# Performance work log

Hardware: AMD Instinct MI355X
Metric: run time of the kernel (lower is better)

The kernel has to match this reference:

```python
import jax, jax.numpy as jnp
import numpy as np

EMBED_DIM = 768
NUM_HEADS = 12
HEAD_DIM = EMBED_DIM // NUM_HEADS


def setup_inputs() -> dict:
    key = jax.random.key(0)
    k_x, k_qkv_w, k_qkv_b, k_pw, k_pb = jax.random.split(key, 5)
    B, S = 16, 1024
    scale = 1.0 / np.sqrt(EMBED_DIM)
    return {
        "x": jax.random.normal(k_x, (B, S, EMBED_DIM), dtype=jnp.float32),
        "qkv_w": jax.random.normal(k_qkv_w, (EMBED_DIM, 3 * EMBED_DIM), dtype=jnp.float32) * scale,
        "qkv_b": jax.random.normal(k_qkv_b, (3 * EMBED_DIM,), dtype=jnp.float32) * 0.02,
        "proj_w": jax.random.normal(k_pw, (EMBED_DIM, EMBED_DIM), dtype=jnp.float32) * scale,
        "proj_b": jax.random.normal(k_pb, (EMBED_DIM,), dtype=jnp.float32) * 0.02,
    }


def reference(x, qkv_w, qkv_b, proj_w, proj_b):
    B, S, E = x.shape
    H, D = NUM_HEADS, HEAD_DIM
    qkv = x @ qkv_w + qkv_b                      # [B, S, 3E]
    qkv = qkv.reshape(B, S, 3, H, D)
    qkv = jnp.transpose(qkv, (2, 0, 3, 1, 4))    # [3, B, H, S, D]
    q, k, v = qkv[0], qkv[1], qkv[2]
    scores = jnp.einsum("bhqd,bhkd->bhqk", q, k) / jnp.sqrt(jnp.float32(D))
    probs = jax.nn.softmax(scores, axis=-1)      # dropout is identity in eval
    attn = jnp.einsum("bhqk,bhkd->bhqd", probs, v)
    attn = jnp.transpose(attn, (0, 2, 1, 3)).reshape(B, S, E)
    return attn @ proj_w + proj_b
```

## Files before the change

### kernel.cpp

```cpp
#include <hip/hip_runtime.h>
#include <hip/hip_bf16.h>

typedef unsigned short u16;
typedef unsigned int u32;
typedef short s16x8 __attribute__((ext_vector_type(8)));
typedef float f32x4 __attribute__((ext_vector_type(4)));

#define EMB 768
#define NH 12
#define HD 64
#define BB 16
#define SS 1024
#define MTOK (BB*SS)
#define NQKV (3*EMB)
#define QSZ ((size_t)BB*NH*SS*HD)

#define GLOBAL_AS const __attribute__((address_space(1))) void*
#define LDS_AS __attribute__((address_space(3))) void*

#if __has_builtin(__builtin_amdgcn_exp2f)
#define EXP2(x) __builtin_amdgcn_exp2f(x)
#else
#define EXP2(x) exp2f(x)
#endif

__device__ __forceinline__ u16 f2bf(float f){
  unsigned u = __float_as_uint(f);
  u += 0x7FFFu + ((u >> 16) & 1u);
  return (u16)(u >> 16);
}
__device__ __forceinline__ u16 f2bf_trunc(float f){
  return (u16)(__float_as_uint(f) >> 16);
}
__device__ __forceinline__ f32x4 mfma16(s16x8 a, s16x8 b, f32x4 c){
  return __builtin_amdgcn_mfma_f32_16x16x32_bf16(a, b, c, 0, 0, 0);
}

#define NBA 12288
#define NBB 1728
#define NBC 576

__device__ __forceinline__ void transpose_body(
    u16 (*tile)[33], const float* __restrict__ in, u16* __restrict__ out,
    int R, int C, int bxi, int byi){
  int bx = bxi * 32, by = byi * 32;
  int tx = threadIdx.x & 31, ty = threadIdx.x >> 5;
  #pragma unroll
  for(int i = 0; i < 32; i += 8)
    tile[ty + i][tx] = f2bf(in[(size_t)(by + ty + i) * C + bx + tx]);
  __syncthreads();
  #pragma unroll
  for(int i = 0; i < 32; i += 8)
    out[(size_t)(bx + ty + i) * R + by + tx] = tile[tx][ty + i];
}

__global__ __launch_bounds__(256) void prep_kernel(
    const float4* __restrict__ x4, ushort4* __restrict__ xb4,
    const float* __restrict__ qkv_w, u16* __restrict__ qkv_wT,
    const float* __restrict__ proj_w, u16* __restrict__ proj_wT){
  __shared__ u16 tile[32][33];
  int bid = blockIdx.x;
  if(bid < NBA){
    int i = bid * 256 + threadIdx.x;
    float4 f = x4[i];
    ushort4 o;
    o.x = f2bf(f.x); o.y = f2bf(f.y); o.z = f2bf(f.z); o.w = f2bf(f.w);
    xb4[i] = o;
  } else if(bid < NBA + NBB){
    int bi = bid - NBA;
    transpose_body(tile, qkv_w, qkv_wT, EMB, NQKV, bi % (NQKV/32), bi / (NQKV/32));
  } else {
    int bi = bid - NBA - NBB;
    transpose_body(tile, proj_w, proj_wT, EMB, EMB, bi % (EMB/32), bi / (EMB/32));
  }
}

__global__ __launch_bounds__(256) void qkv_gemm_kernel(
    const u16* __restrict__ A, const u16* __restrict__ Bt,
    const float* __restrict__ bias,
    u16* __restrict__ Qo, u16* __restrict__ Ko, u16* __restrict__ Vo){
  const int K = 768;
  __shared__ u16 SH[4][128*64];
  u16 (*As)[128*64] = &SH[0];
  u16 (*Bs)[128*64] = &SH[2];
  int tid = threadIdx.x;

  int gx = gridDim.x;
  int nwg = gx * gridDim.y;
  int L = blockIdx.y * gx + blockIdx.x;
  int nl = (L & 7) * (nwg >> 3) + (L >> 3);
  int m0 = (nl / gx) * 128, n0 = (nl % gx) * 128;

  int w = tid >> 6, lane = tid & 63, quad = lane >> 4, l15 = lane & 15;
  int wm = (w >> 1) * 64, wn = (w & 1) * 64;
  int rr = lane >> 3;
  int cp = lane & 7;
  f32x4 acc[4][4] = {};

  auto stage = [&](int p, int k0){
    #pragma unroll
    for(int it = 0; it < 4; ++it){
      int ci = it * 4 + w;
      int r  = ci * 8 + rr;
      int gc = (cp ^ (r & 7)) * 8;
      __builtin_amdgcn_global_load_lds(
          (GLOBAL_AS)(A + (size_t)(m0 + r) * K + k0 + gc),
          (LDS_AS)(As[p] + ci * 512 + lane * 8), 16, 0, 0);
      __builtin_amdgcn_global_load_lds(
          (GLOBAL_AS)(Bt + (size_t)(n0 + r) * K + k0 + gc),
          (LDS_AS)(Bs[p] + ci * 512 + lane * 8), 16, 0, 0);
    }
  };

  stage(0, 0);
  int p = 0;
  for(int k0 = 0; k0 < K; k0 += 64){
    __syncthreads();
    if(k0 + 64 < K) stage(p ^ 1, k0 + 64);
    #pragma unroll
    for(int kk = 0; kk < 2; kk++){
      s16x8 a[4], b[4];
      int ch = ((kk * 4 + quad) ^ (l15 & 7)) * 8;
      #pragma unroll
      for(int i = 0; i < 4; i++){
        a[i] = *(const s16x8*)&As[p][(wm + i*16 + l15) * 64 + ch];
        b[i] = *(const s16x8*)&Bs[p][(wn + i*16 + l15) * 64 + ch];
      }
      #pragma unroll
      for(int mt = 0; mt < 4; mt++)
        #pragma unroll
        for(int nt = 0; nt < 4; nt++)
          acc[mt][nt] = mfma16(a[mt], b[nt], acc[mt][nt]);
    }
    p ^= 1;
  }

  int which = (n0 + wn) / EMB;
  if(which == 2){
    #pragma unroll
    for(int mt = 0; mt < 4; mt++){
      #pragma unroll
      for(int nt = 0; nt < 4; nt++){
        int n = n0 + wn + nt*16 + l15;
        float bv = bias[n];
        int rem = n - 2 * EMB;
        int h = rem >> 6, d = rem & 63;
        int mbase = m0 + wm + mt*16 + quad*4;
        int bb = mbase >> 10, sb = mbase & 1023;
        size_t bh = (size_t)(bb * NH + h);
        ushort4 pk;
        pk.x = f2bf(acc[mt][nt][0] + bv);
        pk.y = f2bf(acc[mt][nt][1] + bv);
        pk.z = f2bf(acc[mt][nt][2] + bv);
        pk.w = f2bf(acc[mt][nt][3] + bv);
        *(ushort4*)&Vo[(bh * HD + d) * SS + sb] = pk;
      }
    }
  } else {
    u16* ep = &SH[0][0];
    __syncthreads();
    #pragma unroll
    for(int mt = 0; mt < 4; mt++){
      #pragma unroll
      for(int nt = 0; nt < 4; nt++){
        int n = n0 + wn + nt*16 + l15;
        float bv = bias[n];
        int row0 = wm + mt*16 + quad*4;
        #pragma unroll
        for(int r = 0; r < 4; r++)
          ep[(row0 + r) * 136 + wn + nt*16 + l15] = f2bf(acc[mt][nt][r] + bv);
      }
    }
    __syncthreads();
    u16* dst = (which == 0) ? Qo : Ko;
    int nb = n0 - which * EMB;
    #pragma unroll
    for(int pass = 0; pass < 8; ++pass){
      int c = pass * 256 + tid;
      int row = c >> 4, chunk = c & 15;
      s16x8 v = *(const s16x8*)&ep[row * 136 + chunk * 8];
      int m = m0 + row;
      int bb = m >> 10, ss = m & 1023;
      int rem = nb + chunk * 8;
      int h = rem >> 6, d = rem & 63;
      size_t bh = (size_t)(bb * NH + h);
      *(s16x8*)&dst[(bh * SS + ss) * HD + d] = v;
    }
  }
}

__global__ __launch_bounds__(512, 2) void proj_gemm_kernel(
    const u16* __restrict__ A, const u16* __restrict__ Bt,
    const float* __restrict__ bias, float* __restrict__ out){
  const int K = 768, NT = 12;
  __shared__ u16 As[2][256*64];
  __shared__ u16 Bs[2][256*64];
  int tid = threadIdx.x;

  int gx = gridDim.x;
  int nwg = gx * gridDim.y;
  int L = blockIdx.y * gx + blockIdx.x;
  int nl = (L & 7) * (nwg >> 3) + (L >> 3);
  int m0 = (nl / gx) * 256, n0 = (nl % gx) * 256;

  int w = tid >> 6, lane = tid & 63, quad = lane >> 4, l15 = lane & 15;
  int wm = (w >> 2) * 128, wn = (w & 3) * 64;
  int rr = lane >> 3;
  int cp = lane & 7;
  f32x4 acc[8][4] = {};

  auto stageQ = [&](int t, int q){
    int d = t & 1, k0 = t * 64;
    const u16* src = (q < 2) ? A : Bt;
    int base = (q < 2) ? m0 : n0;
    u16* dst = (q < 2) ? As[d] : Bs[d];
    int h = q & 1;
    #pragma unroll
    for(int it = 0; it < 2; ++it){
      int ci = h*16 + it*8 + w;
      int r  = ci * 8 + rr;
      int gc = (cp ^ (r & 7)) * 8;
      __builtin_amdgcn_global_load_lds(
          (GLOBAL_AS)(src + (size_t)(base + r) * K + k0 + gc),
          (LDS_AS)(dst + ci * 512 + lane * 8), 16, 0, 0);
    }
  };

  s16x8 a[8], b0[4], b1[4];
  auto dsA = [&](int d, int mh){
    #pragma unroll
    for(int kk = 0; kk < 2; ++kk){
      int ch = ((kk*4 + quad) ^ (l15 & 7)) * 8;
      #pragma unroll
      for(int i = 0; i < 4; ++i)
        a[kk*4+i] = *(const s16x8*)&As[d][(wm + (mh*4+i)*16 + l15) * 64 + ch];
    }
  };
  auto dsB = [&](int d, int nh, s16x8* bb){
    #pragma unroll
    for(int kk = 0; kk < 2; ++kk){
      int ch = ((kk*4 + quad) ^ (l15 & 7)) * 8;
      #pragma unroll
      for(int j = 0; j < 2; ++j)
        bb[kk*2+j] = *(const s16x8*)&Bs[d][(wn + (nh*2+j)*16 + l15) * 64 + ch];
    }
  };
  auto mfmaQ = [&](int mh, int nh, const s16x8* bb){
    __builtin_amdgcn_s_setprio(1);
    #pragma unroll
    for(int kk = 0; kk < 2; ++kk)
      #pragma unroll
      for(int i = 0; i < 4; ++i)
        #pragma unroll
        for(int j = 0; j < 2; ++j)
          acc[mh*4+i][nh*2+j] = mfma16(a[kk*4+i], bb[kk*2+j], acc[mh*4+i][nh*2+j]);
    __builtin_amdgcn_s_setprio(0);
  };

#define PHASE_SYNC() do{ \
    __builtin_amdgcn_s_barrier(); \
    asm volatile("s_waitcnt lgkmcnt(0)" ::: "memory"); \
    __builtin_amdgcn_sched_barrier(0); \
  }while(0)
#define PHASE_END() do{ \
    __builtin_amdgcn_s_barrier(); \
    __builtin_amdgcn_sched_barrier(0); \
  }while(0)

  stageQ(0,0); stageQ(0,1); stageQ(0,2); stageQ(0,3);
  stageQ(1,0);
  asm volatile("s_waitcnt vmcnt(2)" ::: "memory");
  __builtin_amdgcn_s_barrier();
  __builtin_amdgcn_sched_barrier(0);

  #pragma unroll
  for(int j = 0; j < NT/2; ++j){
    int t = 2*j;
    stageQ(t+1, 1);
    dsA(0, 0); dsB(0, 0, b0);
    PHASE_SYNC(); mfmaQ(0, 0, b0); PHASE_END();
    stageQ(t+1, 2);
    dsB(0, 1, b1);
    PHASE_SYNC(); mfmaQ(0, 1, b1); PHASE_END();
    stageQ(t+1, 3);
    dsA(0, 1);
    PHASE_SYNC(); mfmaQ(1, 0, b0); PHASE_END();
    if(t+2 < NT){ stageQ(t+2, 0); asm volatile("s_waitcnt vmcnt(2)" ::: "memory"); }
    else        { asm volatile("s_waitcnt vmcnt(0)" ::: "memory"); }
    PHASE_SYNC(); mfmaQ(1, 1, b1); PHASE_END();
    if(t+2 < NT) stageQ(t+2, 1);
    dsA(1, 0); dsB(1, 0, b0);
    PHASE_SYNC(); mfmaQ(0, 0, b0); PHASE_END();
    if(t+2 < NT) stageQ(t+2, 2);
    dsB(1, 1, b1);
    PHASE_SYNC(); mfmaQ(0, 1, b1); PHASE_END();
    if(t+2 < NT) stageQ(t+2, 3);
    dsA(1, 1);
    PHASE_SYNC(); mfmaQ(1, 0, b0); PHASE_END();
    if(t+3 < NT){ stageQ(t+3, 0); asm volatile("s_waitcnt vmcnt(2)" ::: "memory"); }
    else if(t+2 < NT){ asm volatile("s_waitcnt vmcnt(0)" ::: "memory"); }
    PHASE_SYNC(); mfmaQ(1, 1, b1); PHASE_END();
  }
#undef PHASE_SYNC
#undef PHASE_END

  #pragma unroll
  for(int mt = 0; mt < 8; ++mt){
    #pragma unroll
    for(int nt = 0; nt < 4; ++nt){
      int n = n0 + wn + nt*16 + l15;
      float bv = bias[n];
      #pragma unroll
      for(int r = 0; r < 4; ++r){
        int m = m0 + wm + mt*16 + quad*4 + r;
        out[(size_t)m * EMB + n] = acc[mt][nt][r] + bv;
      }
    }
  }
}

__global__ __launch_bounds__(512) void attn_kernel(
    const u16* __restrict__ Qws, const u16* __restrict__ Kws,
    const u16* __restrict__ Vtws, u16* __restrict__ attn){
  __shared__ u16 Ks[2][64*64];
  __shared__ u16 Vs[2][64*64];
  __shared__ __align__(16) u16 Ps[8][2][16][76];
  int tid = threadIdx.x;
  int w = tid >> 6, lane = tid & 63, quad = lane >> 4, l15 = lane & 15;
  int bh = blockIdx.x;
  int b = bh / NH, h = bh - b * NH;
  int q0 = blockIdx.y * 256 + w * 32;
  const u16* Qbase = Qws  + (size_t)bh * SS * HD;
  const u16* Kbase = Kws  + (size_t)bh * SS * HD;
  const u16* Vbase = Vtws + (size_t)bh * HD * SS;

  s16x8 aq[2][2];
  #pragma unroll
  for(int m = 0; m < 2; m++){
    int qrow = q0 + m*16 + l15;
    #pragma unroll
    for(int kk = 0; kk < 2; kk++)
      aq[m][kk] = *(const s16x8*)(Qbase + (size_t)qrow * HD + kk*32 + quad*8);
  }

  f32x4 o[2][4] = {};
  float psum[2][4] = {};
  const float C1 = 0.125f * 1.44269504f;
  const float C0 = -30.0f * 1.44269504f;

  int krr = lane >> 3, kcp = lane & 7;

  auto stageKV = [&](int p, int kt){
    int ins = w;
    int r   = ins * 8 + krr;
    int gck = (kcp ^ (r & 7)) * 8;
    __builtin_amdgcn_global_load_lds(
        (GLOBAL_AS)(Kbase + (size_t)(kt*64 + r) * HD + gck),
        (LDS_AS)(Ks[p] + ins * 512 + lane * 8), 16, 0, 0);
    __builtin_amdgcn_global_load_lds(
        (GLOBAL_AS)(Vbase + (size_t)r * SS + kt*64 + gck),
        (LDS_AS)(Vs[p] + ins * 512 + lane * 8), 16, 0, 0);
  };

  stageKV(0, 0);
  int p = 0;
  for(int kt = 0; kt < 16; ++kt){
    __syncthreads();
    if(kt < 15) stageKV(p ^ 1, kt + 1);

    #pragma unroll
    for(int nt = 0; nt < 4; ++nt){
      s16x8 bk[2];
      #pragma unroll
      for(int kk = 0; kk < 2; kk++){
        int ch = ((kk*4 + quad) ^ (l15 & 7)) * 8;
        bk[kk] = *(const s16x8*)&Ks[p][(nt*16 + l15) * 64 + ch];
      }
      #pragma unroll
      for(int m = 0; m < 2; m++){
        f32x4 z = {};
        z = mfma16(aq[m][0], bk[0], z);
        z = mfma16(aq[m][1], bk[1], z);
        #pragma unroll
        for(int r = 0; r < 4; r++){
          float pv = EXP2(z[r] * C1 + C0);
          psum[m][r] += pv;
          Ps[w][m][quad*4 + r][nt*16 + l15] = f2bf_trunc(pv);
        }
      }
    }
    #pragma unroll
    for(int k4 = 0; k4 < 2; k4++){
      s16x8 pa[2];
      #pragma unroll
      for(int m = 0; m < 2; m++)
        pa[m] = *(const s16x8*)&Ps[w][m][l15][k4*32 + quad*8];
      #pragma unroll
      for(int nt = 0; nt < 4; nt++){
        int ch = ((k4*4 + quad) ^ (l15 & 7)) * 8;
        s16x8 vb = *(const s16x8*)&Vs[p][(nt*16 + l15) * 64 + ch];
        #pragma unroll
        for(int m = 0; m < 2; m++)
          o[m][nt] = mfma16(pa[m], vb, o[m][nt]);
      }
    }
    p ^= 1;
  }

  #pragma unroll
  for(int m = 0; m < 2; m++){
    #pragma unroll
    for(int r = 0; r < 4; r++){
      float s = psum[m][r];
      s += __shfl_xor(s, 1, 64);
      s += __shfl_xor(s, 2, 64);
      s += __shfl_xor(s, 4, 64);
      s += __shfl_xor(s, 8, 64);
      float inv = 1.0f / s;
      int srow = q0 + m*16 + quad*4 + r;
      size_t base = ((size_t)(b * SS + srow)) * EMB + h * HD;
      #pragma unroll
      for(int nt = 0; nt < 4; nt++)
        attn[base + nt*16 + l15] = f2bf(o[m][nt][r] * inv);
    }
  }
}

extern "C" void kernel_launch(void* const* d_in, const int* in_sizes, int n_in,
                              void* d_out, int out_size, void* d_ws, size_t ws_size,
                              hipStream_t stream){
  const float* x      = (const float*)d_in[0];
  const float* qkv_w  = (const float*)d_in[1];
  const float* qkv_b  = (const float*)d_in[2];
  const float* proj_w = (const float*)d_in[3];
  const float* proj_b = (const float*)d_in[4];

  char* ws = (char*)d_ws;
  u16* qkv_wT  = (u16*)ws; ws += (size_t)NQKV * EMB * 2;
  u16* proj_wT = (u16*)ws; ws += (size_t)EMB * EMB * 2;
  u16* x_bf = (u16*)ws; ws += QSZ * 2;
  u16* Qws  = (u16*)ws; ws += QSZ * 2;
  u16* Kws  = (u16*)ws; ws += QSZ * 2;
  u16* Vtws = (u16*)ws; ws += QSZ * 2;
  u16* attn = x_bf;

  prep_kernel<<<NBA + NBB + NBC, 256, 0, stream>>>(
      (const float4*)x, (ushort4*)x_bf, qkv_w, qkv_wT, proj_w, proj_wT);
  qkv_gemm_kernel<<<dim3(NQKV/128, MTOK/128), 256, 0, stream>>>(
      x_bf, qkv_wT, qkv_b, Qws, Kws, Vtws);
  attn_kernel<<<dim3(BB*NH, SS/256), 512, 0, stream>>>(Qws, Kws, Vtws, attn);
  proj_gemm_kernel<<<dim3(EMB/256, MTOK/256), 512, 0, stream>>>(
      attn, proj_wT, proj_b, (float*)d_out);
}
```

Measured before the change: 277.0 us.

## Shrink proj GEMM to 128x128 tiles with simple double buffer and LDS-staged epilogue

Replaces the 256x256, 512-thread proj GEMM, which used a hand-scheduled 8-phase pipeline, with a 128x128, 256-thread kernel. The new kernel uses a plain double-buffered K loop. The output is staged through LDS in two halves so each fp32 row is written to global memory with coalesced float4 stores. The aim is more workgroups for better CU occupancy and wave balance (768 tiles instead of 192) and cheaper scattered stores. In exchange it loses the finer MFMA/load interleaving and reuses less data per tile.

```diff
diff --git a/kernel.cpp b/kernel.cpp
--- a/kernel.cpp
+++ b/kernel.cpp
@@ -189,132 +189,90 @@
   }
 }
 
-__global__ __launch_bounds__(512, 2) void proj_gemm_kernel(
+__global__ __launch_bounds__(256) void proj_gemm_kernel(
     const u16* __restrict__ A, const u16* __restrict__ Bt,
     const float* __restrict__ bias, float* __restrict__ out){
-  const int K = 768, NT = 12;
-  __shared__ u16 As[2][256*64];
-  __shared__ u16 Bs[2][256*64];
+  const int K = 768;
+  __shared__ u16 SH[4][128*64];
+  u16 (*As)[128*64] = &SH[0];
+  u16 (*Bs)[128*64] = &SH[2];
   int tid = threadIdx.x;
 
   int gx = gridDim.x;
   int nwg = gx * gridDim.y;
   int L = blockIdx.y * gx + blockIdx.x;
   int nl = (L & 7) * (nwg >> 3) + (L >> 3);
-  int m0 = (nl / gx) * 256, n0 = (nl % gx) * 256;
+  int m0 = (nl / gx) * 128, n0 = (nl % gx) * 128;
 
   int w = tid >> 6, lane = tid & 63, quad = lane >> 4, l15 = lane & 15;
-  int wm = (w >> 2) * 128, wn = (w & 3) * 64;
+  int wm = (w >> 1) * 64, wn = (w & 1) * 64;
   int rr = lane >> 3;
   int cp = lane & 7;
-  f32x4 acc[8][4] = {};
-
-  auto stageQ = [&](int t, int q){
-    int d = t & 1, k0 = t * 64;
-    const u16* src = (q < 2) ? A : Bt;
-    int base = (q < 2) ? m0 : n0;
-    u16* dst = (q < 2) ? As[d] : Bs[d];
-    int h = q & 1;
-    #pragma unroll
-    for(int it = 0; it < 2; ++it){
-      int ci = h*16 + it*8 + w;
+  f32x4 acc[4][4] = {};
+
+  auto stage = [&](int p, int k0){
+    #pragma unroll
+    for(int it = 0; it < 4; ++it){
+      int ci = it * 4 + w;
       int r  = ci * 8 + rr;
       int gc = (cp ^ (r & 7)) * 8;
       __builtin_amdgcn_global_load_lds(
-          (GLOBAL_AS)(src + (size_t)(base + r) * K + k0 + gc),
-          (LDS_AS)(dst + ci * 512 + lane * 8), 16, 0, 0);
+          (GLOBAL_AS)(A + (size_t)(m0 + r) * K + k0 + gc),
+          (LDS_AS)(As[p] + ci * 512 + lane * 8), 16, 0, 0);
+      __builtin_amdgcn_global_load_lds(
+          (GLOBAL_AS)(Bt + (size_t)(n0 + r) * K + k0 + gc),
+          (LDS_AS)(Bs[p] + ci * 512 + lane * 8), 16, 0, 0);
     }
   };
 
-  s16x8 a[8], b0[4], b1[4];
-  auto dsA = [&](int d, int mh){
-    #pragma unroll
-    for(int kk = 0; kk < 2; ++kk){
-      int ch = ((kk*4 + quad) ^ (l15 & 7)) * 8;
-      #pragma unroll
-      for(int i = 0; i < 4; ++i)
-        a[kk*4+i] = *(const s16x8*)&As[d][(wm + (mh*4+i)*16 + l15) * 64 + ch];
-    }
-  };
-  auto dsB = [&](int d, int nh, s16x8* bb){
-    #pragma unroll
-    for(int kk = 0; kk < 2; ++kk){
-      int ch = ((kk*4 + quad) ^ (l15 & 7)) * 8;
-      #pragma unroll
-      for(int j = 0; j < 2; ++j)
-        bb[kk*2+j] = *(const s16x8*)&Bs[d][(wn + (nh*2+j)*16 + l15) * 64 + ch];
-    }
-  };
-  auto mfmaQ = [&](int mh, int nh, const s16x8* bb){
-    __builtin_amdgcn_s_setprio(1);
-    #pragma unroll
-    for(int kk = 0; kk < 2; ++kk)
-      #pragma unroll
-      for(int i = 0; i < 4; ++i)
-        #pragma unroll
-        for(int j = 0; j < 2; ++j)
-          acc[mh*4+i][nh*2+j] = mfma16(a[kk*4+i], bb[kk*2+j], acc[mh*4+i][nh*2+j]);
-    __builtin_amdgcn_s_setprio(0);
-  };
-
-#define PHASE_SYNC() do{ \
-    __builtin_amdgcn_s_barrier(); \
-    asm volatile("s_waitcnt lgkmcnt(0)" ::: "memory"); \
-    __builtin_amdgcn_sched_barrier(0); \
-  }while(0)
-#define PHASE_END() do{ \
-    __builtin_amdgcn_s_barrier(); \
-    __builtin_amdgcn_sched_barrier(0); \
-  }while(0)
-
-  stageQ(0,0); stageQ(0,1); stageQ(0,2); stageQ(0,3);
-  stageQ(1,0);
-  asm volatile("s_waitcnt vmcnt(2)" ::: "memory");
-  __builtin_amdgcn_s_barrier();
-  __builtin_amdgcn_sched_barrier(0);
-
+  stage(0, 0);
+  int p = 0;
+  for(int k0 = 0; k0 < K; k0 += 64){
+    __syncthreads();
+    if(k0 + 64 < K) stage(p ^ 1, k0 + 64);
+    #pragma unroll
+    for(int kk = 0; kk < 2; kk++){
+      s16x8 a[4], b[4];
+      int ch = ((kk * 4 + quad) ^ (l15 & 7)) * 8;
+      #pragma unroll
+      for(int i = 0; i < 4; i++){
+        a[i] = *(const s16x8*)&As[p][(wm + i*16 + l15) * 64 + ch];
+        b[i] = *(const s16x8*)&Bs[p][(wn + i*16 + l15) * 64 + ch];
+      }
+      #pragma unroll
+      for(int mt = 0; mt < 4; mt++)
+        #pragma unroll
+        for(int nt = 0; nt < 4; nt++)
+          acc[mt][nt] = mfma16(a[mt], b[nt], acc[mt][nt]);
+    }
+    p ^= 1;
+  }
+
+  float* epf = (float*)&SH[0][0];
+  int myhalf = wm >> 6;
   #pragma unroll
-  for(int j = 0; j < NT/2; ++j){
-    int t = 2*j;
-    stageQ(t+1, 1);
-    dsA(0, 0); dsB(0, 0, b0);
-    PHASE_SYNC(); mfmaQ(0, 0, b0); PHASE_END();
-    stageQ(t+1, 2);
-    dsB(0, 1, b1);
-    PHASE_SYNC(); mfmaQ(0, 1, b1); PHASE_END();
-    stageQ(t+1, 3);
-    dsA(0, 1);
-    PHASE_SYNC(); mfmaQ(1, 0, b0); PHASE_END();
-    if(t+2 < NT){ stageQ(t+2, 0); asm volatile("s_waitcnt vmcnt(2)" ::: "memory"); }
-    else        { asm volatile("s_waitcnt vmcnt(0)" ::: "memory"); }
-    PHASE_SYNC(); mfmaQ(1, 1, b1); PHASE_END();
-    if(t+2 < NT) stageQ(t+2, 1);
-    dsA(1, 0); dsB(1, 0, b0);
-    PHASE_SYNC(); mfmaQ(0, 0, b0); PHASE_END();
-    if(t+2 < NT) stageQ(t+2, 2);
-    dsB(1, 1, b1);
-    PHASE_SYNC(); mfmaQ(0, 1, b1); PHASE_END();
-    if(t+2 < NT) stageQ(t+2, 3);
-    dsA(1, 1);
-    PHASE_SYNC(); mfmaQ(1, 0, b0); PHASE_END();
-    if(t+3 < NT){ stageQ(t+3, 0); asm volatile("s_waitcnt vmcnt(2)" ::: "memory"); }
-    else if(t+2 < NT){ asm volatile("s_waitcnt vmcnt(0)" ::: "memory"); }
-    PHASE_SYNC(); mfmaQ(1, 1, b1); PHASE_END();
-  }
-#undef PHASE_SYNC
-#undef PHASE_END
-
-  #pragma unroll
-  for(int mt = 0; mt < 8; ++mt){
-    #pragma unroll
-    for(int nt = 0; nt < 4; ++nt){
-      int n = n0 + wn + nt*16 + l15;
-      float bv = bias[n];
-      #pragma unroll
-      for(int r = 0; r < 4; ++r){
-        int m = m0 + wm + mt*16 + quad*4 + r;
-        out[(size_t)m * EMB + n] = acc[mt][nt][r] + bv;
-      }
+  for(int h = 0; h < 2; ++h){
+    __syncthreads();
+    if(myhalf == h){
+      #pragma unroll
+      for(int mt = 0; mt < 4; mt++){
+        #pragma unroll
+        for(int nt = 0; nt < 4; nt++){
+          float bv = bias[n0 + wn + nt*16 + l15];
+          int row0 = mt*16 + quad*4;
+          #pragma unroll
+          for(int r = 0; r < 4; r++)
+            epf[(row0 + r) * 132 + wn + nt*16 + l15] = acc[mt][nt][r] + bv;
+        }
+      }
+    }
+    __syncthreads();
+    #pragma unroll
+    for(int pass = 0; pass < 8; ++pass){
+      int c = pass * 256 + tid;
+      int row = c >> 5, ch = c & 31;
+      float4 v = *(const float4*)&epf[row * 132 + ch * 4];
+      *(float4*)&out[(size_t)(m0 + h*64 + row) * EMB + n0 + ch * 4] = v;
     }
   }
 }
@@ -449,6 +407,6 @@
   qkv_gemm_kernel<<<dim3(NQKV/128, MTOK/128), 256, 0, stream>>>(
       x_bf, qkv_wT, qkv_b, Qws, Kws, Vtws);
   attn_kernel<<<dim3(BB*NH, SS/256), 512, 0, stream>>>(Qws, Kws, Vtws, attn);
-  proj_gemm_kernel<<<dim3(EMB/256, MTOK/256), 512, 0, stream>>>(
+  proj_gemm_kernel<<<dim3(EMB/128, MTOK/128), 256, 0, stream>>>(
       attn, proj_wT, proj_b, (float*)d_out);
 }
```

After: 288.5 us. +4.1%, slower.
